# Optimization experiments

Hardware: AMD Instinct MI355X
Metric: run time of the kernel (lower is better)

## Reference

```python
import jax, jax.numpy as jnp
import numpy as np

B, S, P, J = 32, 128, 2, 17
DIN, DOUT, DRNN, DHID = 2, 3, 128, 256
N = P * J
DT = 0.1   # delta_t from init
K = 4      # Euler steps, hardcoded k=int(4) in source


def setup_inputs() -> dict:
    key = jax.random.key(0)
    ks = jax.random.split(key, 12)
    g = lambda k, sh, fan: (jax.random.normal(k, sh, jnp.float32) / np.sqrt(fan)).astype(jnp.float32)
    d = {}
    d['x2d'] = jax.random.normal(ks[0], (B, S, P, J, DIN), jnp.float32)
    d['mask'] = jax.random.randint(ks[1], (B, S, P, J, 1), 0, 2).astype(jnp.int32)
    # ODE MLP: DRNN -> DHID -> DHID -> DRNN (num_hidden=2 hidden layers, tanh)
    d['ode_w0'] = g(ks[2], (DRNN, DHID), DRNN); d['ode_b0'] = jnp.zeros((DHID,), jnp.float32)
    d['ode_w1'] = g(ks[3], (DHID, DHID), DHID); d['ode_b1'] = jnp.zeros((DHID,), jnp.float32)
    d['ode_w2'] = g(ks[4], (DHID, DRNN), DHID); d['ode_b2'] = jnp.zeros((DRNN,), jnp.float32)
    # GRU cell 0: input DIN -> hidden DRNN ; GRU cell 1: input DRNN -> hidden DRNN
    d['wih0'] = g(ks[5], (DIN, 3 * DRNN), DIN);  d['whh0'] = g(ks[6], (DRNN, 3 * DRNN), DRNN)
    d['bih0'] = jnp.zeros((3 * DRNN,), jnp.float32); d['bhh0'] = jnp.zeros((3 * DRNN,), jnp.float32)
    d['wih1'] = g(ks[7], (DRNN, 3 * DRNN), DRNN); d['whh1'] = g(ks[8], (DRNN, 3 * DRNN), DRNN)
    d['bih1'] = jnp.zeros((3 * DRNN,), jnp.float32); d['bhh1'] = jnp.zeros((3 * DRNN,), jnp.float32)
    d['wout'] = g(ks[9], (DRNN, DOUT), DRNN); d['bout'] = jnp.zeros((DOUT,), jnp.float32)
    d['h0'] = 0.01 * jax.random.normal(ks[10], (1, 1, DRNN), jnp.float32)
    return d


def _ode(h, w0, b0, w1, b1, w2, b2):
    h = jnp.tanh(h @ w0 + b0)
    h = jnp.tanh(h @ w1 + b1)
    return h @ w2 + b2


def _gru(x, h, wih, whh, bih, bhh):
    gi = x @ wih + bih
    gh = h @ whh + bhh
    ir, iz, ig = jnp.split(gi, 3, axis=-1)
    hr, hz, hg = jnp.split(gh, 3, axis=-1)
    r = jax.nn.sigmoid(ir + hr)
    z = jax.nn.sigmoid(iz + hz)
    n = jnp.tanh(ig + r * hg)
    return (1.0 - z) * n + z * h


def reference(x2d, mask, ode_w0, ode_b0, ode_w1, ode_b1, ode_w2, ode_b2,
              wih0, whh0, bih0, bhh0, wih1, whh1, bih1, bhh1, wout, bout, h0):
    m = mask.astype(x2d.dtype)                      # (B,S,P,J,1)
    xs = (x2d * m).reshape(B, S, N, DIN)            # masked 2D input
    ms = m.reshape(B, S, N, 1)
    h_init = jnp.broadcast_to(h0, (B, N, DRNN))

    def step(h, inp):
        x, mm = inp                                 # (B,N,DIN), (B,N,1)
        h1 = h
        for _ in range(K):                          # 4 Euler ODE steps
            h1 = h1 + DT * _ode(h1, ode_w0, ode_b0, ode_w1, ode_b1, ode_w2, ode_b2)
        h2 = _gru(x, h1, wih0, whh0, bih0, bhh0)    # stacked GRU, both conditioned on h1
        h2 = _gru(h2, h1, wih1, whh1, bih1, bhh1)
        h_next = h1 * (1.0 - mm) + h2 * mm
        return h_next, h1

    _, hs = jax.lax.scan(step, h_init,
                         (jnp.swapaxes(xs, 0, 1), jnp.swapaxes(ms, 0, 1)))
    hs = jnp.swapaxes(hs, 0, 1)                     # (B,S,N,DRNN)
    ys = (hs @ wout + bout).reshape(B, S, P, J, DOUT)
    return ys
```

## Files before the change

### kernel.cpp

```cpp
#include <hip/hip_runtime.h>

typedef _Float16 f16x8 __attribute__((ext_vector_type(8)));
typedef float f32x4 __attribute__((ext_vector_type(4)));

constexpr int S_ = 128;
constexpr float DT_ = 0.1f;
constexpr float LS = 2048.0f;
constexpr float INV = 1.0f / 2048.0f;

#define MFMA(a, b, c) __builtin_amdgcn_mfma_f32_16x16x32_f16((a), (b), (c), 0, 0, 0)

#define OB0   0
#define OB1   256
#define OB2   512
#define OBHH0 640
#define OBIH0 1024
#define OBIH1 1408
#define OBHH1 1792
#define NBIAS 2176

__device__ __forceinline__ float fast_tanh(float x) {
    float e = __expf(2.0f * x);
    return 1.0f - 2.0f / (e + 1.0f);
}
__device__ __forceinline__ float fast_sigmoid(float x) {
    return 1.0f / (1.0f + __expf(-x));
}
__device__ __forceinline__ f32x4 bc4(float v) { return (f32x4){v, v, v, v}; }

__global__ void prep_hl(const float* __restrict__ src, _Float16* __restrict__ hi,
                        _Float16* __restrict__ lo, int K, int N) {
    int e = blockIdx.x * 256 + threadIdx.x;
    if (e >= K * N) return;
    int tile = e >> 9, r = e & 511;
    int lane = r >> 3, j = r & 7;
    int KT = K >> 5;
    int nt = tile / KT, kt = tile - nt * KT;
    int k = kt * 32 + ((lane >> 4) << 3) + j;
    int n = nt * 16 + (lane & 15);
    float v = src[k * N + n];
    _Float16 h = (_Float16)v;
    hi[e] = h;
    lo[e] = (_Float16)((v - (float)h) * LS);
}

template<int KT>
__device__ __forceinline__ f32x4 tile_mm(
    const _Float16* __restrict__ Wh, const _Float16* __restrict__ Wl, int nt,
    const _Float16* __restrict__ Ah, const _Float16* __restrict__ Al, int lda,
    int l, int lrow, int lk8, float bias)
{
    const _Float16* ph = Wh + ((size_t)nt * KT) * 512 + l * 8;
    const _Float16* pl = Wl + ((size_t)nt * KT) * 512 + l * 8;
    f16x8 bh[KT], bl[KT];
#pragma unroll
    for (int kt = 0; kt < KT; ++kt) {
        bh[kt] = *(const f16x8*)(ph + kt * 512);
        bl[kt] = *(const f16x8*)(pl + kt * 512);
    }
    f32x4 acc = bc4(bias), pe = bc4(0.f), qe = bc4(0.f);
#pragma unroll
    for (int kt = 0; kt < KT; ++kt) {
        f16x8 ah = *(const f16x8*)(Ah + lrow * lda + kt * 32 + lk8);
        f16x8 al = *(const f16x8*)(Al + lrow * lda + kt * 32 + lk8);
        acc = MFMA(ah, bh[kt], acc);
        pe  = MFMA(ah, bl[kt], pe);
        qe  = MFMA(al, bh[kt], qe);
    }
    return acc + (pe + qe) * INV;
}

__global__ __launch_bounds__(512, 1) void odernn_mfma(
    const float* __restrict__ x2d, const int* __restrict__ maskp,
    const _Float16* __restrict__ w0h, const _Float16* __restrict__ w0l,
    const _Float16* __restrict__ w1hg, const _Float16* __restrict__ w1lg,
    const _Float16* __restrict__ w2h, const _Float16* __restrict__ w2l,
    const _Float16* __restrict__ hh0h, const _Float16* __restrict__ hh0l,
    const _Float16* __restrict__ ih1h, const _Float16* __restrict__ ih1l,
    const _Float16* __restrict__ hh1h, const _Float16* __restrict__ hh1l,
    const float* __restrict__ b0, const float* __restrict__ b1,
    const float* __restrict__ b2, const float* __restrict__ bhh0,
    const float* __restrict__ bih0, const float* __restrict__ wih0,
    const float* __restrict__ bih1, const float* __restrict__ bhh1,
    const float* __restrict__ wout, const float* __restrict__ bout,
    const float* __restrict__ h0, float* __restrict__ out)
{
    __shared__ float hF[16][128];
    __shared__ _Float16 bAh[16][264], bAl[16][264];
    __shared__ _Float16 bBh[16][264], bBl[16][264];
    __shared__ _Float16 bHh[16][136], bHl[16][136];
    __shared__ float sbias[NBIAS];
    __shared__ float swi0[768];
    __shared__ float swout[384];
    __shared__ float sbout[4];
    __shared__ float sx0[16], sx1[16], smm[16];
    __shared__ int sIdx[16];

    const int tid = (int)threadIdx.x;
    const int wv = tid >> 6;
    const int l = tid & 63;
    const int lrow = l & 15;
    const int lk8 = (l >> 4) << 3;
    const int rbase = (l >> 4) << 2;

    for (int e = tid; e < 256; e += 512) { sbias[OB0 + e] = b0[e]; sbias[OB1 + e] = b1[e]; }
    for (int e = tid; e < 128; e += 512) sbias[OB2 + e] = b2[e];
    for (int e = tid; e < 384; e += 512) {
        sbias[OBHH0 + e] = bhh0[e];
        sbias[OBIH0 + e] = bih0[e];
        sbias[OBIH1 + e] = bih1[e];
        sbias[OBHH1 + e] = bhh1[e];
        swout[e] = wout[e];
    }
    for (int e = tid; e < 768; e += 512) swi0[e] = wih0[e];
    if (tid < 3) sbout[tid] = bout[tid];
    for (int e = tid; e < 2048; e += 512) {
        int row = e >> 7, col = e & 127;
        float v = h0[col];
        hF[row][col] = v;
        _Float16 hh = (_Float16)v;
        bHh[row][col] = hh;
        bHl[row][col] = (_Float16)((v - (float)hh) * LS);
    }
    if (tid < 16) {
        int grow = (int)blockIdx.x * 16 + tid;
        int bb = grow / 34, nn = grow - bb * 34;
        sIdx[tid] = bb * (S_ * 34) + nn;
    }
    __syncthreads();

    for (int s = 0; s < S_; ++s) {
        if (tid < 16) {
            int idx = sIdx[tid] + s * 34;
            float fm = (float)maskp[idx];
            smm[tid] = fm;
            sx0[tid] = x2d[2 * idx] * fm;
            sx1[tid] = x2d[2 * idx + 1] * fm;
        }

        for (int it = 0; it < 4; ++it) {
            {
                f32x4 v0 = tile_mm<4>(w0h, w0l, wv, &bHh[0][0], &bHl[0][0], 136,
                                      l, lrow, lk8, sbias[OB0 + (wv << 4) + lrow]);
                f32x4 v1 = tile_mm<4>(w0h, w0l, wv + 8, &bHh[0][0], &bHl[0][0], 136,
                                      l, lrow, lk8, sbias[OB0 + ((wv + 8) << 4) + lrow]);
                const int n0 = wv << 4, n1 = (wv + 8) << 4;
#pragma unroll
                for (int r = 0; r < 4; ++r) {
                    int row = rbase + r;
                    float t0 = fast_tanh(v0[r]);
                    float t1 = fast_tanh(v1[r]);
                    _Float16 hh = (_Float16)t0;
                    bBh[row][n0 + lrow] = hh;
                    bBl[row][n0 + lrow] = (_Float16)((t0 - (float)hh) * LS);
                    hh = (_Float16)t1;
                    bBh[row][n1 + lrow] = hh;
                    bBl[row][n1 + lrow] = (_Float16)((t1 - (float)hh) * LS);
                }
            }
            __syncthreads();

            {
                f32x4 v0 = tile_mm<8>(w1hg, w1lg, wv, &bBh[0][0], &bBl[0][0], 264,
                                      l, lrow, lk8, sbias[OB1 + (wv << 4) + lrow]);
                f32x4 v1 = tile_mm<8>(w1hg, w1lg, wv + 8, &bBh[0][0], &bBl[0][0], 264,
                                      l, lrow, lk8, sbias[OB1 + ((wv + 8) << 4) + lrow]);
                const int n0 = wv << 4, n1 = (wv + 8) << 4;
#pragma unroll
                for (int r = 0; r < 4; ++r) {
                    int row = rbase + r;
                    float t0 = fast_tanh(v0[r]);
                    float t1 = fast_tanh(v1[r]);
                    _Float16 hh = (_Float16)t0;
                    bAh[row][n0 + lrow] = hh;
                    bAl[row][n0 + lrow] = (_Float16)((t0 - (float)hh) * LS);
                    hh = (_Float16)t1;
                    bAh[row][n1 + lrow] = hh;
                    bAl[row][n1 + lrow] = (_Float16)((t1 - (float)hh) * LS);
                }
            }
            __syncthreads();

            {
                f32x4 f = tile_mm<8>(w2h, w2l, wv, &bAh[0][0], &bAl[0][0], 264,
                                     l, lrow, lk8, sbias[OB2 + (wv << 4) + lrow]);
#pragma unroll
                for (int r = 0; r < 4; ++r) {
                    int row = rbase + r, col = (wv << 4) + lrow;
                    float v = hF[row][col] + DT_ * f[r];
                    hF[row][col] = v;
                    _Float16 hh = (_Float16)v;
                    bHh[row][col] = hh;
                    bHl[row][col] = (_Float16)((v - (float)hh) * LS);
                }
            }
            __syncthreads();
        }

        {
            f32x4 gh[3];
#pragma unroll
            for (int t = 0; t < 3; ++t)
                gh[t] = tile_mm<4>(hh0h, hh0l, wv + (t << 3), &bHh[0][0], &bHl[0][0], 136,
                                   l, lrow, lk8, sbias[OBHH0 + ((wv + (t << 3)) << 4) + lrow]);
            {
                int yrow = wv + ((l >> 5) << 3);
                int ll = l & 31;
                int c0 = ll << 2;
                float4 hv = *(const float4*)&hF[yrow][c0];
                float y0 = hv.x * swout[c0 * 3] + hv.y * swout[(c0 + 1) * 3] +
                           hv.z * swout[(c0 + 2) * 3] + hv.w * swout[(c0 + 3) * 3];
                float y1 = hv.x * swout[c0 * 3 + 1] + hv.y * swout[(c0 + 1) * 3 + 1] +
                           hv.z * swout[(c0 + 2) * 3 + 1] + hv.w * swout[(c0 + 3) * 3 + 1];
                float y2 = hv.x * swout[c0 * 3 + 2] + hv.y * swout[(c0 + 1) * 3 + 2] +
                           hv.z * swout[(c0 + 2) * 3 + 2] + hv.w * swout[(c0 + 3) * 3 + 2];
#pragma unroll
                for (int m = 16; m >= 1; m >>= 1) {
                    y0 += __shfl_xor(y0, m, 64);
                    y1 += __shfl_xor(y1, m, 64);
                    y2 += __shfl_xor(y2, m, 64);
                }
                if (ll == 0) {
                    int idx = sIdx[yrow] + s * 34;
                    out[idx * 3 + 0] = y0 + sbout[0];
                    out[idx * 3 + 1] = y1 + sbout[1];
                    out[idx * 3 + 2] = y2 + sbout[2];
                }
            }
            {
                int col = (wv << 4) + lrow;
                float wxr0 = swi0[col], wxr1 = swi0[384 + col];
                float wxz0 = swi0[128 + col], wxz1 = swi0[384 + 128 + col];
                float wxn0 = swi0[256 + col], wxn1 = swi0[384 + 256 + col];
                float bir = sbias[OBIH0 + col], biz = sbias[OBIH0 + 128 + col], bin = sbias[OBIH0 + 256 + col];
#pragma unroll
                for (int r = 0; r < 4; ++r) {
                    int row = rbase + r;
                    float xa = sx0[row], xb = sx1[row];
                    float rg = fast_sigmoid(bir + xa * wxr0 + xb * wxr1 + gh[0][r]);
                    float zg = fast_sigmoid(biz + xa * wxz0 + xb * wxz1 + gh[1][r]);
                    float nn = fast_tanh(bin + xa * wxn0 + xb * wxn1 + rg * gh[2][r]);
                    float h1 = hF[row][col];
                    float h2 = (1.0f - zg) * nn + zg * h1;
                    _Float16 hh = (_Float16)h2;
                    bBh[row][col] = hh;
                    bBl[row][col] = (_Float16)((h2 - (float)hh) * LS);
                }
            }
        }
        __syncthreads();

        {
            f32x4 gi[3], gh[3];
#pragma unroll
            for (int t = 0; t < 3; ++t)
                gi[t] = tile_mm<4>(ih1h, ih1l, wv + (t << 3), &bBh[0][0], &bBl[0][0], 264,
                                   l, lrow, lk8, sbias[OBIH1 + ((wv + (t << 3)) << 4) + lrow]);
#pragma unroll
            for (int t = 0; t < 3; ++t)
                gh[t] = tile_mm<4>(hh1h, hh1l, wv + (t << 3), &bHh[0][0], &bHl[0][0], 136,
                                   l, lrow, lk8, sbias[OBHH1 + ((wv + (t << 3)) << 4) + lrow]);

            __syncthreads();
#pragma unroll
            for (int r = 0; r < 4; ++r) {
                int row = rbase + r, col = (wv << 4) + lrow;
                float rg = fast_sigmoid(gi[0][r] + gh[0][r]);
                float zg = fast_sigmoid(gi[1][r] + gh[1][r]);
                float nn = fast_tanh(gi[2][r] + rg * gh[2][r]);
                float h1 = hF[row][col];
                float h2 = (1.0f - zg) * nn + zg * h1;
                float v = (smm[row] != 0.0f) ? h2 : h1;
                hF[row][col] = v;
                _Float16 hh = (_Float16)v;
                bHh[row][col] = hh;
                bHl[row][col] = (_Float16)((v - (float)hh) * LS);
            }
        }
        __syncthreads();
    }
}

extern "C" void kernel_launch(void* const* d_in, const int* in_sizes, int n_in,
                              void* d_out, int out_size, void* d_ws, size_t ws_size,
                              hipStream_t stream) {
    const float* x2d  = (const float*)d_in[0];
    const int*   mask = (const int*)d_in[1];
    const float* w0   = (const float*)d_in[2];
    const float* b0   = (const float*)d_in[3];
    const float* w1   = (const float*)d_in[4];
    const float* b1   = (const float*)d_in[5];
    const float* w2   = (const float*)d_in[6];
    const float* b2   = (const float*)d_in[7];
    const float* wih0 = (const float*)d_in[8];
    const float* whh0 = (const float*)d_in[9];
    const float* bih0 = (const float*)d_in[10];
    const float* bhh0 = (const float*)d_in[11];
    const float* wih1 = (const float*)d_in[12];
    const float* whh1 = (const float*)d_in[13];
    const float* bih1 = (const float*)d_in[14];
    const float* bhh1 = (const float*)d_in[15];
    const float* wout = (const float*)d_in[16];
    const float* bout = (const float*)d_in[17];
    const float* h0   = (const float*)d_in[18];
    float* out = (float*)d_out;

    _Float16* base = (_Float16*)d_ws;
    _Float16* pw0h  = base;
    _Float16* pw1h  = base + 32768;
    _Float16* pw2h  = base + 98304;
    _Float16* ph0h  = base + 131072;
    _Float16* pi1h  = base + 180224;
    _Float16* ph1h  = base + 229376;
    _Float16* lobase = base + 278528;
    _Float16* pw0l  = lobase;
    _Float16* pw1l  = lobase + 32768;
    _Float16* pw2l  = lobase + 98304;
    _Float16* ph0l  = lobase + 131072;
    _Float16* pi1l  = lobase + 180224;
    _Float16* ph1l  = lobase + 229376;

    hipLaunchKernelGGL(prep_hl, dim3(128), dim3(256), 0, stream, w0,   pw0h, pw0l, 128, 256);
    hipLaunchKernelGGL(prep_hl, dim3(256), dim3(256), 0, stream, w1,   pw1h, pw1l, 256, 256);
    hipLaunchKernelGGL(prep_hl, dim3(128), dim3(256), 0, stream, w2,   pw2h, pw2l, 256, 128);
    hipLaunchKernelGGL(prep_hl, dim3(192), dim3(256), 0, stream, whh0, ph0h, ph0l, 128, 384);
    hipLaunchKernelGGL(prep_hl, dim3(192), dim3(256), 0, stream, wih1, pi1h, pi1l, 128, 384);
    hipLaunchKernelGGL(prep_hl, dim3(192), dim3(256), 0, stream, whh1, ph1h, ph1l, 128, 384);

    hipLaunchKernelGGL(odernn_mfma, dim3(68), dim3(512), 0, stream,
        x2d, mask, pw0h, pw0l, pw1h, pw1l, pw2h, pw2l,
        ph0h, ph0l, pi1h, pi1l, ph1h, ph1l,
        b0, b1, b2, bhh0, bih0, wih0, bih1, bhh1, wout, bout, h0, out);
}
```

Before: 6.895 ms.

## Split rows across more blocks, four real rows per block, zero-padded MFMA tiles

Each block now handles 4 sequence rows instead of 16, and the grid grows from 68 to 272 blocks so more compute units work through the sequential recurrence at once. The 16-row MFMA tiles are kept, with rows 4-15 zero-padded and their write-backs masked. Latency per step should stay about the same while more CUs are used, but MFMA work is wasted on padding rows and each block reads the full weight set from global memory or L2.

```diff
diff --git a/kernel.cpp b/kernel.cpp
--- a/kernel.cpp
+++ b/kernel.cpp
@@ -4,6 +4,7 @@
 typedef float f32x4 __attribute__((ext_vector_type(4)));
 
 constexpr int S_ = 128;
+constexpr int NRB = 4;
 constexpr float DT_ = 0.1f;
 constexpr float LS = 2048.0f;
 constexpr float INV = 1.0f / 2048.0f;
@@ -85,7 +86,7 @@
     const float* __restrict__ wout, const float* __restrict__ bout,
     const float* __restrict__ h0, float* __restrict__ out)
 {
-    __shared__ float hF[16][128];
+    __shared__ float hF[NRB][128];
     __shared__ _Float16 bAh[16][264], bAl[16][264];
     __shared__ _Float16 bBh[16][264], bBl[16][264];
     __shared__ _Float16 bHh[16][136], bHl[16][136];
@@ -93,8 +94,8 @@
     __shared__ float swi0[768];
     __shared__ float swout[384];
     __shared__ float sbout[4];
-    __shared__ float sx0[16], sx1[16], smm[16];
-    __shared__ int sIdx[16];
+    __shared__ float sx0[NRB], sx1[NRB], smm[NRB];
+    __shared__ int sIdx[NRB];
 
     const int tid = (int)threadIdx.x;
     const int wv = tid >> 6;
@@ -114,23 +115,27 @@
     }
     for (int e = tid; e < 768; e += 512) swi0[e] = wih0[e];
     if (tid < 3) sbout[tid] = bout[tid];
-    for (int e = tid; e < 2048; e += 512) {
-        int row = e >> 7, col = e & 127;
-        float v = h0[col];
-        hF[row][col] = v;
+    for (int e = tid; e < 16 * 264; e += 512) {
+        bAh[0][e] = (_Float16)0.f; bAl[0][e] = (_Float16)0.f;
+        bBh[0][e] = (_Float16)0.f; bBl[0][e] = (_Float16)0.f;
+    }
+    for (int e = tid; e < 16 * 136; e += 512) {
+        int row = e / 136, col = e - row * 136;
+        float v = (col < 128) ? h0[col] : 0.f;
         _Float16 hh = (_Float16)v;
-        bHh[row][col] = hh;
-        bHl[row][col] = (_Float16)((v - (float)hh) * LS);
-    }
-    if (tid < 16) {
-        int grow = (int)blockIdx.x * 16 + tid;
+        bHh[0][e] = hh;
+        bHl[0][e] = (_Float16)((v - (float)hh) * LS);
+    }
+    for (int e = tid; e < NRB * 128; e += 512) hF[e >> 7][e & 127] = h0[e & 127];
+    if (tid < NRB) {
+        int grow = (int)blockIdx.x * NRB + tid;
         int bb = grow / 34, nn = grow - bb * 34;
         sIdx[tid] = bb * (S_ * 34) + nn;
     }
     __syncthreads();
 
     for (int s = 0; s < S_; ++s) {
-        if (tid < 16) {
+        if (tid < NRB) {
             int idx = sIdx[tid] + s * 34;
             float fm = (float)maskp[idx];
             smm[tid] = fm;
@@ -148,14 +153,16 @@
 #pragma unroll
                 for (int r = 0; r < 4; ++r) {
                     int row = rbase + r;
-                    float t0 = fast_tanh(v0[r]);
-                    float t1 = fast_tanh(v1[r]);
-                    _Float16 hh = (_Float16)t0;
-                    bBh[row][n0 + lrow] = hh;
-                    bBl[row][n0 + lrow] = (_Float16)((t0 - (float)hh) * LS);
-                    hh = (_Float16)t1;
-                    bBh[row][n1 + lrow] = hh;
-                    bBl[row][n1 + lrow] = (_Float16)((t1 - (float)hh) * LS);
+                    if (row < NRB) {
+                        float t0 = fast_tanh(v0[r]);
+                        float t1 = fast_tanh(v1[r]);
+                        _Float16 hh = (_Float16)t0;
+                        bBh[row][n0 + lrow] = hh;
+                        bBl[row][n0 + lrow] = (_Float16)((t0 - (float)hh) * LS);
+                        hh = (_Float16)t1;
+                        bBh[row][n1 + lrow] = hh;
+                        bBl[row][n1 + lrow] = (_Float16)((t1 - (float)hh) * LS);
+                    }
                 }
             }
             __syncthreads();
@@ -169,14 +176,16 @@
 #pragma unroll
                 for (int r = 0; r < 4; ++r) {
                     int row = rbase + r;
-                    float t0 = fast_tanh(v0[r]);
-                    float t1 = fast_tanh(v1[r]);
-                    _Float16 hh = (_Float16)t0;
-                    bAh[row][n0 + lrow] = hh;
-                    bAl[row][n0 + lrow] = (_Float16)((t0 - (float)hh) * LS);
-                    hh = (_Float16)t1;
-                    bAh[row][n1 + lrow] = hh;
-                    bAl[row][n1 + lrow] = (_Float16)((t1 - (float)hh) * LS);
+                    if (row < NRB) {
+                        float t0 = fast_tanh(v0[r]);
+                        float t1 = fast_tanh(v1[r]);
+                        _Float16 hh = (_Float16)t0;
+                        bAh[row][n0 + lrow] = hh;
+                        bAl[row][n0 + lrow] = (_Float16)((t0 - (float)hh) * LS);
+                        hh = (_Float16)t1;
+                        bAh[row][n1 + lrow] = hh;
+                        bAl[row][n1 + lrow] = (_Float16)((t1 - (float)hh) * LS);
+                    }
                 }
             }
             __syncthreads();
@@ -186,12 +195,15 @@
                                      l, lrow, lk8, sbias[OB2 + (wv << 4) + lrow]);
 #pragma unroll
                 for (int r = 0; r < 4; ++r) {
-                    int row = rbase + r, col = (wv << 4) + lrow;
-                    float v = hF[row][col] + DT_ * f[r];
-                    hF[row][col] = v;
-                    _Float16 hh = (_Float16)v;
-                    bHh[row][col] = hh;
-                    bHl[row][col] = (_Float16)((v - (float)hh) * LS);
+                    int row = rbase + r;
+                    if (row < NRB) {
+                        int col = (wv << 4) + lrow;
+                        float v = hF[row][col] + DT_ * f[r];
+                        hF[row][col] = v;
+                        _Float16 hh = (_Float16)v;
+                        bHh[row][col] = hh;
+                        bHl[row][col] = (_Float16)((v - (float)hh) * LS);
+                    }
                 }
             }
             __syncthreads();
@@ -207,7 +219,9 @@
                 int yrow = wv + ((l >> 5) << 3);
                 int ll = l & 31;
                 int c0 = ll << 2;
-                float4 hv = *(const float4*)&hF[yrow][c0];
+                float4 hv;
+                if (yrow < NRB) hv = *(const float4*)&hF[yrow][c0];
+                else hv = make_float4(0.f, 0.f, 0.f, 0.f);
                 float y0 = hv.x * swout[c0 * 3] + hv.y * swout[(c0 + 1) * 3] +
                            hv.z * swout[(c0 + 2) * 3] + hv.w * swout[(c0 + 3) * 3];
                 float y1 = hv.x * swout[c0 * 3 + 1] + hv.y * swout[(c0 + 1) * 3 + 1] +
@@ -220,7 +234,7 @@
                     y1 += __shfl_xor(y1, m, 64);
                     y2 += __shfl_xor(y2, m, 64);
                 }
-                if (ll == 0) {
+                if (ll == 0 && yrow < NRB) {
                     int idx = sIdx[yrow] + s * 34;
                     out[idx * 3 + 0] = y0 + sbout[0];
                     out[idx * 3 + 1] = y1 + sbout[1];
@@ -236,15 +250,17 @@
 #pragma unroll
                 for (int r = 0; r < 4; ++r) {
                     int row = rbase + r;
-                    float xa = sx0[row], xb = sx1[row];
-                    float rg = fast_sigmoid(bir + xa * wxr0 + xb * wxr1 + gh[0][r]);
-                    float zg = fast_sigmoid(biz + xa * wxz0 + xb * wxz1 + gh[1][r]);
-                    float nn = fast_tanh(bin + xa * wxn0 + xb * wxn1 + rg * gh[2][r]);
-                    float h1 = hF[row][col];
-                    float h2 = (1.0f - zg) * nn + zg * h1;
-                    _Float16 hh = (_Float16)h2;
-                    bBh[row][col] = hh;
-                    bBl[row][col] = (_Float16)((h2 - (float)hh) * LS);
+                    if (row < NRB) {
+                        float xa = sx0[row], xb = sx1[row];
+                        float rg = fast_sigmoid(bir + xa * wxr0 + xb * wxr1 + gh[0][r]);
+                        float zg = fast_sigmoid(biz + xa * wxz0 + xb * wxz1 + gh[1][r]);
+                        float nn = fast_tanh(bin + xa * wxn0 + xb * wxn1 + rg * gh[2][r]);
+                        float h1 = hF[row][col];
+                        float h2 = (1.0f - zg) * nn + zg * h1;
+                        _Float16 hh = (_Float16)h2;
+                        bBh[row][col] = hh;
+                        bBl[row][col] = (_Float16)((h2 - (float)hh) * LS);
+                    }
                 }
             }
         }
@@ -264,17 +280,20 @@
             __syncthreads();
 #pragma unroll
             for (int r = 0; r < 4; ++r) {
-                int row = rbase + r, col = (wv << 4) + lrow;
-                float rg = fast_sigmoid(gi[0][r] + gh[0][r]);
-                float zg = fast_sigmoid(gi[1][r] + gh[1][r]);
-                float nn = fast_tanh(gi[2][r] + rg * gh[2][r]);
-                float h1 = hF[row][col];
-                float h2 = (1.0f - zg) * nn + zg * h1;
-                float v = (smm[row] != 0.0f) ? h2 : h1;
-                hF[row][col] = v;
-                _Float16 hh = (_Float16)v;
-                bHh[row][col] = hh;
-                bHl[row][col] = (_Float16)((v - (float)hh) * LS);
+                int row = rbase + r;
+                if (row < NRB) {
+                    int col = (wv << 4) + lrow;
+                    float rg = fast_sigmoid(gi[0][r] + gh[0][r]);
+                    float zg = fast_sigmoid(gi[1][r] + gh[1][r]);
+                    float nn = fast_tanh(gi[2][r] + rg * gh[2][r]);
+                    float h1 = hF[row][col];
+                    float h2 = (1.0f - zg) * nn + zg * h1;
+                    float v = (smm[row] != 0.0f) ? h2 : h1;
+                    hF[row][col] = v;
+                    _Float16 hh = (_Float16)v;
+                    bHh[row][col] = hh;
+                    bHl[row][col] = (_Float16)((v - (float)hh) * LS);
+                }
             }
         }
         __syncthreads();
@@ -327,7 +346,7 @@
     hipLaunchKernelGGL(prep_hl, dim3(192), dim3(256), 0, stream, wih1, pi1h, pi1l, 128, 384);
     hipLaunchKernelGGL(prep_hl, dim3(192), dim3(256), 0, stream, whh1, ph1h, ph1l, 128, 384);
 
-    hipLaunchKernelGGL(odernn_mfma, dim3(68), dim3(512), 0, stream,
+    hipLaunchKernelGGL(odernn_mfma, dim3(272), dim3(512), 0, stream,
         x2d, mask, pw0h, pw0l, pw1h, pw1l, pw2h, pw2l,
         ph0h, ph0l, pi1h, pi1l, ph1h, ph1l,
         b0, b1, b2, bhh0, bih0, wih0, bih1, bhh1, wout, bout, h0, out);
```

Measured after the change: 16.60 ms. 2.41x slower.

## Stream weight tiles through LDS with double-buffered global_load_lds prefetch

Applied to the files above, without the earlier changes.

Previously each wave loaded all of a weight tile's K-slices into registers straight from global memory before running its MFMAs. Now each wave streams hi/lo weight fragments into a private double-buffered LDS staging area using global_load_lds. Each k-slice's fetch is issued while the previous slice is being multiplied, with explicit vmcnt waits and scheduling barriers. The aim is to hide global/L2 latency and lower register pressure, at the cost of extra LDS traffic and more waits per phase.

```diff
diff --git a/kernel.cpp b/kernel.cpp
--- a/kernel.cpp
+++ b/kernel.cpp
@@ -9,6 +9,7 @@
 constexpr float INV = 1.0f / 2048.0f;
 
 #define MFMA(a, b, c) __builtin_amdgcn_mfma_f32_16x16x32_f16((a), (b), (c), 0, 0, 0)
+#define SB() __builtin_amdgcn_sched_barrier(0)
 
 #define OB0   0
 #define OB1   256
@@ -27,6 +28,18 @@
     return 1.0f / (1.0f + __expf(-x));
 }
 __device__ __forceinline__ f32x4 bc4(float v) { return (f32x4){v, v, v, v}; }
+
+__device__ __forceinline__ void gld16(const _Float16* g, _Float16* l) {
+    __builtin_amdgcn_global_load_lds(
+        (const __attribute__((address_space(1))) void*)g,
+        (__attribute__((address_space(3))) void*)l, 16, 0, 0);
+}
+template<int N> __device__ __forceinline__ void waitvm() {
+    if constexpr (N == 0) asm volatile("s_waitcnt vmcnt(0)" ::: "memory");
+    else if constexpr (N == 2) asm volatile("s_waitcnt vmcnt(2)" ::: "memory");
+    else if constexpr (N == 4) asm volatile("s_waitcnt vmcnt(4)" ::: "memory");
+    SB();
+}
 
 __global__ void prep_hl(const float* __restrict__ src, _Float16* __restrict__ hi,
                         _Float16* __restrict__ lo, int K, int N) {
@@ -44,30 +57,47 @@
     lo[e] = (_Float16)((v - (float)h) * LS);
 }
 
-template<int KT>
-__device__ __forceinline__ f32x4 tile_mm(
-    const _Float16* __restrict__ Wh, const _Float16* __restrict__ Wl, int nt,
+template<int KT, int NTW>
+__device__ __forceinline__ void mm_phase(
+    const _Float16* __restrict__ Wh, const _Float16* __restrict__ Wl,
+    const int* nts,
     const _Float16* __restrict__ Ah, const _Float16* __restrict__ Al, int lda,
-    int l, int lrow, int lk8, float bias)
+    _Float16* wbase, int l, int lrow, int lk8,
+    f32x4* acc, f32x4* pe, f32x4* qe)
 {
-    const _Float16* ph = Wh + ((size_t)nt * KT) * 512 + l * 8;
-    const _Float16* pl = Wl + ((size_t)nt * KT) * 512 + l * 8;
-    f16x8 bh[KT], bl[KT];
+    waitvm<0>();
+    const int lb = l * 8;
+#pragma unroll
+    for (int t = 0; t < NTW; ++t) {
+        gld16(Wh + ((size_t)nts[t] * KT) * 512 + lb, wbase + (2 * t) * 512);
+        gld16(Wl + ((size_t)nts[t] * KT) * 512 + lb, wbase + (2 * t + 1) * 512);
+    }
 #pragma unroll
     for (int kt = 0; kt < KT; ++kt) {
-        bh[kt] = *(const f16x8*)(ph + kt * 512);
-        bl[kt] = *(const f16x8*)(pl + kt * 512);
-    }
-    f32x4 acc = bc4(bias), pe = bc4(0.f), qe = bc4(0.f);
-#pragma unroll
-    for (int kt = 0; kt < KT; ++kt) {
+        _Float16* cb = wbase + (kt & 1) * 2048;
+        if (kt + 1 < KT) {
+            SB();
+            _Float16* nb = wbase + ((kt + 1) & 1) * 2048;
+#pragma unroll
+            for (int t = 0; t < NTW; ++t) {
+                gld16(Wh + ((size_t)(nts[t] * KT + kt + 1)) * 512 + lb, nb + (2 * t) * 512);
+                gld16(Wl + ((size_t)(nts[t] * KT + kt + 1)) * 512 + lb, nb + (2 * t + 1) * 512);
+            }
+            waitvm<2 * NTW>();
+        } else {
+            waitvm<0>();
+        }
         f16x8 ah = *(const f16x8*)(Ah + lrow * lda + kt * 32 + lk8);
         f16x8 al = *(const f16x8*)(Al + lrow * lda + kt * 32 + lk8);
-        acc = MFMA(ah, bh[kt], acc);
-        pe  = MFMA(ah, bl[kt], pe);
-        qe  = MFMA(al, bh[kt], qe);
-    }
-    return acc + (pe + qe) * INV;
+#pragma unroll
+        for (int t = 0; t < NTW; ++t) {
+            f16x8 bh = *(const f16x8*)(cb + (2 * t) * 512 + lb);
+            f16x8 bl = *(const f16x8*)(cb + (2 * t + 1) * 512 + lb);
+            acc[t] = MFMA(ah, bh, acc[t]);
+            pe[t]  = MFMA(ah, bl, pe[t]);
+            qe[t]  = MFMA(al, bh, qe[t]);
+        }
+    }
 }
 
 __global__ __launch_bounds__(512, 1) void odernn_mfma(
@@ -89,6 +119,7 @@
     __shared__ _Float16 bAh[16][264], bAl[16][264];
     __shared__ _Float16 bBh[16][264], bBl[16][264];
     __shared__ _Float16 bHh[16][136], bHl[16][136];
+    __shared__ _Float16 wstage[8][2][4][512];
     __shared__ float sbias[NBIAS];
     __shared__ float swi0[768];
     __shared__ float swout[384];
@@ -102,6 +133,7 @@
     const int lrow = l & 15;
     const int lk8 = (l >> 4) << 3;
     const int rbase = (l >> 4) << 2;
+    _Float16* wb = &wstage[wv][0][0][0];
 
     for (int e = tid; e < 256; e += 512) { sbias[OB0 + e] = b0[e]; sbias[OB1 + e] = b1[e]; }
     for (int e = tid; e < 128; e += 512) sbias[OB2 + e] = b2[e];
@@ -129,6 +161,10 @@
     }
     __syncthreads();
 
+    const int nts01[2] = {wv, wv + 8};
+    const int nts2[1] = {wv + 16};
+    const int ntsw[1] = {wv};
+
     for (int s = 0; s < S_; ++s) {
         if (tid < 16) {
             int idx = sIdx[tid] + s * 34;
@@ -140,54 +176,58 @@
 
         for (int it = 0; it < 4; ++it) {
             {
-                f32x4 v0 = tile_mm<4>(w0h, w0l, wv, &bHh[0][0], &bHl[0][0], 136,
-                                      l, lrow, lk8, sbias[OB0 + (wv << 4) + lrow]);
-                f32x4 v1 = tile_mm<4>(w0h, w0l, wv + 8, &bHh[0][0], &bHl[0][0], 136,
-                                      l, lrow, lk8, sbias[OB0 + ((wv + 8) << 4) + lrow]);
+                f32x4 acc[2] = {bc4(sbias[OB0 + (wv << 4) + lrow]),
+                                bc4(sbias[OB0 + ((wv + 8) << 4) + lrow])};
+                f32x4 pe[2] = {bc4(0.f), bc4(0.f)}, qe[2] = {bc4(0.f), bc4(0.f)};
+                mm_phase<4, 2>(w0h, w0l, nts01, &bHh[0][0], &bHl[0][0], 136,
+                               wb, l, lrow, lk8, acc, pe, qe);
                 const int n0 = wv << 4, n1 = (wv + 8) << 4;
 #pragma unroll
                 for (int r = 0; r < 4; ++r) {
                     int row = rbase + r;
-                    float t0 = fast_tanh(v0[r]);
-                    float t1 = fast_tanh(v1[r]);
-                    _Float16 hh = (_Float16)t0;
+                    float v0 = fast_tanh(acc[0][r] + (pe[0][r] + qe[0][r]) * INV);
+                    float v1 = fast_tanh(acc[1][r] + (pe[1][r] + qe[1][r]) * INV);
+                    _Float16 hh = (_Float16)v0;
                     bBh[row][n0 + lrow] = hh;
-                    bBl[row][n0 + lrow] = (_Float16)((t0 - (float)hh) * LS);
-                    hh = (_Float16)t1;
+                    bBl[row][n0 + lrow] = (_Float16)((v0 - (float)hh) * LS);
+                    hh = (_Float16)v1;
                     bBh[row][n1 + lrow] = hh;
-                    bBl[row][n1 + lrow] = (_Float16)((t1 - (float)hh) * LS);
+                    bBl[row][n1 + lrow] = (_Float16)((v1 - (float)hh) * LS);
                 }
             }
             __syncthreads();
 
             {
-                f32x4 v0 = tile_mm<8>(w1hg, w1lg, wv, &bBh[0][0], &bBl[0][0], 264,
-                                      l, lrow, lk8, sbias[OB1 + (wv << 4) + lrow]);
-                f32x4 v1 = tile_mm<8>(w1hg, w1lg, wv + 8, &bBh[0][0], &bBl[0][0], 264,
-                                      l, lrow, lk8, sbias[OB1 + ((wv + 8) << 4) + lrow]);
+                f32x4 acc[2] = {bc4(sbias[OB1 + (wv << 4) + lrow]),
+                                bc4(sbias[OB1 + ((wv + 8) << 4) + lrow])};
+                f32x4 pe[2] = {bc4(0.f), bc4(0.f)}, qe[2] = {bc4(0.f), bc4(0.f)};
+                mm_phase<8, 2>(w1hg, w1lg, nts01, &bBh[0][0], &bBl[0][0], 264,
+                               wb, l, lrow, lk8, acc, pe, qe);
                 const int n0 = wv << 4, n1 = (wv + 8) << 4;
 #pragma unroll
                 for (int r = 0; r < 4; ++r) {
                     int row = rbase + r;
-                    float t0 = fast_tanh(v0[r]);
-                    float t1 = fast_tanh(v1[r]);
-                    _Float16 hh = (_Float16)t0;
+                    float v0 = fast_tanh(acc[0][r] + (pe[0][r] + qe[0][r]) * INV);
+                    float v1 = fast_tanh(acc[1][r] + (pe[1][r] + qe[1][r]) * INV);
+                    _Float16 hh = (_Float16)v0;
                     bAh[row][n0 + lrow] = hh;
-                    bAl[row][n0 + lrow] = (_Float16)((t0 - (float)hh) * LS);
-                    hh = (_Float16)t1;
+                    bAl[row][n0 + lrow] = (_Float16)((v0 - (float)hh) * LS);
+                    hh = (_Float16)v1;
                     bAh[row][n1 + lrow] = hh;
-                    bAl[row][n1 + lrow] = (_Float16)((t1 - (float)hh) * LS);
+                    bAl[row][n1 + lrow] = (_Float16)((v1 - (float)hh) * LS);
                 }
             }
             __syncthreads();
 
             {
-                f32x4 f = tile_mm<8>(w2h, w2l, wv, &bAh[0][0], &bAl[0][0], 264,
-                                     l, lrow, lk8, sbias[OB2 + (wv << 4) + lrow]);
+                f32x4 acc[1] = {bc4(sbias[OB2 + (wv << 4) + lrow])};
+                f32x4 pe[1] = {bc4(0.f)}, qe[1] = {bc4(0.f)};
+                mm_phase<8, 1>(w2h, w2l, ntsw, &bAh[0][0], &bAl[0][0], 264,
+                               wb, l, lrow, lk8, acc, pe, qe);
 #pragma unroll
                 for (int r = 0; r < 4; ++r) {
                     int row = rbase + r, col = (wv << 4) + lrow;
-                    float v = hF[row][col] + DT_ * f[r];
+                    float v = hF[row][col] + DT_ * (acc[0][r] + (pe[0][r] + qe[0][r]) * INV);
                     hF[row][col] = v;
                     _Float16 hh = (_Float16)v;
                     bHh[row][col] = hh;
@@ -198,11 +238,15 @@
         }
 
         {
-            f32x4 gh[3];
-#pragma unroll
-            for (int t = 0; t < 3; ++t)
-                gh[t] = tile_mm<4>(hh0h, hh0l, wv + (t << 3), &bHh[0][0], &bHl[0][0], 136,
-                                   l, lrow, lk8, sbias[OBHH0 + ((wv + (t << 3)) << 4) + lrow]);
+            f32x4 acc[3] = {bc4(sbias[OBHH0 + (wv << 4) + lrow]),
+                            bc4(sbias[OBHH0 + ((wv + 8) << 4) + lrow]),
+                            bc4(sbias[OBHH0 + ((wv + 16) << 4) + lrow])};
+            f32x4 pe[3] = {bc4(0.f), bc4(0.f), bc4(0.f)};
+            f32x4 qe[3] = {bc4(0.f), bc4(0.f), bc4(0.f)};
+            mm_phase<4, 2>(hh0h, hh0l, nts01, &bHh[0][0], &bHl[0][0], 136,
+                           wb, l, lrow, lk8, acc, pe, qe);
+            mm_phase<4, 1>(hh0h, hh0l, nts2, &bHh[0][0], &bHl[0][0], 136,
+                           wb, l, lrow, lk8, acc + 2, pe + 2, qe + 2);
             {
                 int yrow = wv + ((l >> 5) << 3);
                 int ll = l & 31;
@@ -237,9 +281,10 @@
                 for (int r = 0; r < 4; ++r) {
                     int row = rbase + r;
                     float xa = sx0[row], xb = sx1[row];
-                    float rg = fast_sigmoid(bir + xa * wxr0 + xb * wxr1 + gh[0][r]);
-                    float zg = fast_sigmoid(biz + xa * wxz0 + xb * wxz1 + gh[1][r]);
-                    float nn = fast_tanh(bin + xa * wxn0 + xb * wxn1 + rg * gh[2][r]);
+                    float rg = fast_sigmoid(bir + xa * wxr0 + xb * wxr1 + acc[0][r] + (pe[0][r] + qe[0][r]) * INV);
+                    float zg = fast_sigmoid(biz + xa * wxz0 + xb * wxz1 + acc[1][r] + (pe[1][r] + qe[1][r]) * INV);
+                    float gn = acc[2][r] + (pe[2][r] + qe[2][r]) * INV;
+                    float nn = fast_tanh(bin + xa * wxn0 + xb * wxn1 + rg * gn);
                     float h1 = hF[row][col];
                     float h2 = (1.0f - zg) * nn + zg * h1;
                     _Float16 hh = (_Float16)h2;
@@ -251,23 +296,39 @@
         __syncthreads();
 
         {
-            f32x4 gi[3], gh[3];
-#pragma unroll
-            for (int t = 0; t < 3; ++t)
-                gi[t] = tile_mm<4>(ih1h, ih1l, wv + (t << 3), &bBh[0][0], &bBl[0][0], 264,
-                                   l, lrow, lk8, sbias[OBIH1 + ((wv + (t << 3)) << 4) + lrow]);
-#pragma unroll
-            for (int t = 0; t < 3; ++t)
-                gh[t] = tile_mm<4>(hh1h, hh1l, wv + (t << 3), &bHh[0][0], &bHl[0][0], 136,
-                                   l, lrow, lk8, sbias[OBHH1 + ((wv + (t << 3)) << 4) + lrow]);
+            f32x4 aI[3] = {bc4(sbias[OBIH1 + (wv << 4) + lrow]),
+                           bc4(sbias[OBIH1 + ((wv + 8) << 4) + lrow]),
+                           bc4(sbias[OBIH1 + ((wv + 16) << 4) + lrow])};
+            f32x4 pI[3] = {bc4(0.f), bc4(0.f), bc4(0.f)};
+            f32x4 qI[3] = {bc4(0.f), bc4(0.f), bc4(0.f)};
+            mm_phase<4, 2>(ih1h, ih1l, nts01, &bBh[0][0], &bBl[0][0], 264,
+                           wb, l, lrow, lk8, aI, pI, qI);
+            mm_phase<4, 1>(ih1h, ih1l, nts2, &bBh[0][0], &bBl[0][0], 264,
+                           wb, l, lrow, lk8, aI + 2, pI + 2, qI + 2);
+            f32x4 gi0 = aI[0] + (pI[0] + qI[0]) * INV;
+            f32x4 gi1 = aI[1] + (pI[1] + qI[1]) * INV;
+            f32x4 gi2 = aI[2] + (pI[2] + qI[2]) * INV;
+
+            f32x4 aH[3] = {bc4(sbias[OBHH1 + (wv << 4) + lrow]),
+                           bc4(sbias[OBHH1 + ((wv + 8) << 4) + lrow]),
+                           bc4(sbias[OBHH1 + ((wv + 16) << 4) + lrow])};
+            f32x4 pH[3] = {bc4(0.f), bc4(0.f), bc4(0.f)};
+            f32x4 qH[3] = {bc4(0.f), bc4(0.f), bc4(0.f)};
+            mm_phase<4, 2>(hh1h, hh1l, nts01, &bHh[0][0], &bHl[0][0], 136,
+                           wb, l, lrow, lk8, aH, pH, qH);
+            mm_phase<4, 1>(hh1h, hh1l, nts2, &bHh[0][0], &bHl[0][0], 136,
+                           wb, l, lrow, lk8, aH + 2, pH + 2, qH + 2);
 
             __syncthreads();
 #pragma unroll
             for (int r = 0; r < 4; ++r) {
                 int row = rbase + r, col = (wv << 4) + lrow;
-                float rg = fast_sigmoid(gi[0][r] + gh[0][r]);
-                float zg = fast_sigmoid(gi[1][r] + gh[1][r]);
-                float nn = fast_tanh(gi[2][r] + rg * gh[2][r]);
+                float ghr = aH[0][r] + (pH[0][r] + qH[0][r]) * INV;
+                float ghz = aH[1][r] + (pH[1][r] + qH[1][r]) * INV;
+                float ghn = aH[2][r] + (pH[2][r] + qH[2][r]) * INV;
+                float rg = fast_sigmoid(gi0[r] + ghr);
+                float zg = fast_sigmoid(gi1[r] + ghz);
+                float nn = fast_tanh(gi2[r] + rg * ghn);
                 float h1 = hF[row][col];
                 float h2 = (1.0f - zg) * nn + zg * h1;
                 float v = (smm[row] != 0.0f) ? h2 : h1;
```

New measurement: 7.287 ms. 1.06x slower.
